# Kernel optimization log

Measured on AMD Instinct MI355X. Metric: run time of the kernel, lower is better.

The kernel has to match this reference:

```python
import jax, jax.numpy as jnp
import numpy as np

B, S, E, H = 4, 2048, 1024, 16
D = E // H  # head_dim = 64


def setup_inputs() -> dict:
    key = jax.random.key(0)
    k1, k2, k3, k4, k5 = jax.random.split(key, 5)
    # xavier_uniform bounds
    lim_qkv = float(np.sqrt(6.0 / (E + 3 * E)))
    lim_out = float(np.sqrt(6.0 / (E + E)))
    return {
        "inp": jax.random.normal(k1, (B, S, E), dtype=jnp.float32),
        "qkv_w": jax.random.uniform(k2, (3 * E, E), minval=-lim_qkv, maxval=lim_qkv, dtype=jnp.float32),
        "qkv_b": jnp.zeros((3 * E,), dtype=jnp.float32),
        "out_w": jax.random.uniform(k3, (E, E), minval=-lim_out, maxval=lim_out, dtype=jnp.float32),
        "out_b": jnp.zeros((E,), dtype=jnp.float32),
    }


def reference(inp, qkv_w, qkv_b, out_w, out_b):
    b, s, _ = inp.shape
    # qkv projection: [b,s,3E]
    qkv = jnp.einsum("bse,fe->bsf", inp, qkv_w) + qkv_b
    qkv = qkv.reshape(b, s, 3, H, D).transpose(2, 0, 3, 1, 4)  # [3,b,h,s,d]
    q, k, v = qkv[0], qkv[1], qkv[2]
    scale = 1.0 / jnp.sqrt(jnp.float32(D))
    scores = jnp.einsum("bhqd,bhkd->bhqk", q, k) * scale
    attn = jax.nn.softmax(scores, axis=-1)  # dropout = identity (eval mode)
    ctx = jnp.einsum("bhqk,bhkd->bhqd", attn, v)
    ctx = ctx.transpose(0, 2, 1, 3).reshape(b, s, E)
    out = jnp.einsum("bse,fe->bsf", ctx, out_w) + out_b
    return out
```

## Files before the change

### kernel.cpp

```cpp
#include <hip/hip_runtime.h>
#include <stdint.h>

typedef unsigned short u16;
typedef __bf16 bf16x8 __attribute__((ext_vector_type(8)));
typedef float f32x4 __attribute__((ext_vector_type(4)));
typedef float f32x16 __attribute__((ext_vector_type(16)));

#define DEV static __device__ __forceinline__

DEV u16 f2bf(float f) {
  uint32_t u = __float_as_uint(f);
  u += 0x7fffu + ((u >> 16) & 1u);
  return (u16)(u >> 16);
}

DEV void g2l16(const void* g, void* l) {
  __builtin_amdgcn_global_load_lds(
      (__attribute__((address_space(1))) void*)(g),
      (__attribute__((address_space(3))) void*)(l), 16, 0, 0);
}

DEV f32x4 mfma16(bf16x8 a, bf16x8 b, f32x4 c) {
  return __builtin_amdgcn_mfma_f32_16x16x32_bf16(a, b, c, 0, 0, 0);
}
DEV f32x16 mfma32(bf16x8 a, bf16x8 b, f32x16 c) {
  return __builtin_amdgcn_mfma_f32_32x32x16_bf16(a, b, c, 0, 0, 0);
}

DEV bf16x8 lds_ld(const char* p) { return *(const bf16x8*)p; }

DEV float fexp2(float x) {
  float r;
  asm("v_exp_f32 %0, %1" : "=v"(r) : "v"(x));
  return r;
}

DEV uint32_t cvtpk(float lo, float hi) {
  uint32_t r;
  asm("v_cvt_pk_bf16_f32 %0, %1, %2" : "=v"(r) : "v"(lo), "v"(hi));
  return r;
}
DEV void pswap(uint32_t& a, uint32_t& b) {
  auto r = __builtin_amdgcn_permlane32_swap((int)a, (int)b, false, false);
  a = (uint32_t)r[0];
  b = (uint32_t)r[1];
}
DEV float xhalf_sum(float x) {
  auto r = __builtin_amdgcn_permlane32_swap(__float_as_int(x), __float_as_int(x), false, false);
  return __int_as_float(r[0]) + __int_as_float(r[1]);
}

__global__ __launch_bounds__(256) void cvt_kernel(const float* __restrict__ in,
                                                  u16* __restrict__ out, int n4) {
  int i = blockIdx.x * 256 + threadIdx.x;
  if (i >= n4) return;
  float4 v = ((const float4*)in)[i];
  ushort4 o;
  o.x = f2bf(v.x); o.y = f2bf(v.y); o.z = f2bf(v.z); o.w = f2bf(v.w);
  ((ushort4*)out)[i] = o;
}

template<int EPI>
__global__ __launch_bounds__(256, 2) void gemm_bt(
    const u16* __restrict__ A, const u16* __restrict__ B,
    const float* __restrict__ bias, void* __restrict__ C,
    u16* __restrict__ vT,
    int M, int N, int K, int qcols, float qscale, int vcol0) {
  __shared__ char sm[2][32768];
  const int tid = threadIdx.x;
  const int w = tid >> 6, l = tid & 63;
  const int wr = w >> 1, wc = w & 1;
  const int bm0 = blockIdx.x * 128, bn0 = blockIdx.y * 128;
  const int lr = l >> 3, lsl = (l & 7) ^ lr;
  const u16* gA = A + (size_t)(bm0 + w * 32 + lr) * K + lsl * 8;
  const u16* gB = B + (size_t)(bn0 + w * 32 + lr) * K + lsl * 8;

  auto stage = [&](int t, int pp) {
    char* ba = sm[pp] + w * 32 * 128;
    char* bb = ba + 16384;
    const u16* a = gA + t * 64;
    const u16* b = gB + t * 64;
#pragma unroll
    for (int i = 0; i < 4; ++i) {
      g2l16(a + (size_t)i * 8 * K, ba + i * 8 * 128);
      g2l16(b + (size_t)i * 8 * K, bb + i * 8 * 128);
    }
  };

  f32x4 acc[4][4] = {};
  const int NT = K / 64;
  int pp = 0;
  stage(0, 0);
  __syncthreads();
  for (int t = 0; t < NT; ++t) {
    if (t + 1 < NT) stage(t + 1, pp ^ 1);
    const char* bufA = sm[pp];
    const char* bufB = bufA + 16384;
#pragma unroll
    for (int ks = 0; ks < 2; ++ks) {
      bf16x8 af[4], bfr[4];
#pragma unroll
      for (int i = 0; i < 4; ++i) {
        const int rowA = wr * 64 + i * 16 + (l & 15);
        const int colb = (ks * 64 + ((l >> 4) << 4)) ^ ((rowA & 7) << 4);
        af[i] = lds_ld(bufA + rowA * 128 + colb);
        const int rowB = wc * 64 + i * 16 + (l & 15);
        bfr[i] = lds_ld(bufB + rowB * 128 + colb);
      }
#pragma unroll
      for (int i = 0; i < 4; ++i)
#pragma unroll
        for (int j = 0; j < 4; ++j)
          acc[i][j] = mfma16(af[i], bfr[j], acc[i][j]);
    }
    __syncthreads();
    pp ^= 1;
  }
  const int cr = (l >> 4) * 4, cc = l & 15;
  if (EPI == 1 && bn0 >= vcol0) {
#pragma unroll
    for (int i = 0; i < 4; ++i) {
      const int gr = bm0 + wr * 64 + i * 16 + cr;
      const int b = gr >> 11, s = gr & 2047;
#pragma unroll
      for (int j = 0; j < 4; ++j) {
        const int gc = bn0 + wc * 64 + j * 16 + cc;
        const float bv = bias[gc];
        const int vc = gc - vcol0;
        u16* dst = vT + ((size_t)((b * 16 + (vc >> 6)) * 64 + (vc & 63))) * 2048 + s;
        ushort4 pk;
        pk.x = f2bf(acc[i][j][0] + bv);
        pk.y = f2bf(acc[i][j][1] + bv);
        pk.z = f2bf(acc[i][j][2] + bv);
        pk.w = f2bf(acc[i][j][3] + bv);
        *(ushort4*)dst = pk;
      }
    }
    return;
  }
#pragma unroll
  for (int i = 0; i < 4; ++i) {
    const int gr = bm0 + wr * 64 + i * 16 + cr;
#pragma unroll
    for (int j = 0; j < 4; ++j) {
      const int gc = bn0 + wc * 64 + j * 16 + cc;
      const float bv = bias[gc];
      const float scl = (gc < qcols) ? qscale : 1.0f;
#pragma unroll
      for (int r = 0; r < 4; ++r) {
        const float v = (acc[i][j][r] + bv) * scl;
        if (EPI == 0) ((float*)C)[(size_t)(gr + r) * N + gc] = v;
        else          ((u16*)C)[(size_t)(gr + r) * N + gc] = f2bf(v);
      }
    }
  }
}

__global__ __launch_bounds__(256, 2) void attn(const u16* __restrict__ qkv,
                                               const u16* __restrict__ vT,
                                               u16* __restrict__ ctx) {
  constexpr int S = 2048, E = 1024, TE = 3072, NT = S / 64;
  const int id = blockIdx.x;
  const int x = id & 7, j = id >> 3;
  const int bh = x * 8 + (j & 7), qt = j >> 3;
  const int b = bh >> 4, h = bh & 15;
  const int tid = threadIdx.x, w = tid >> 6, l = tid & 63;
  const int q = l & 31, hi = l >> 5;
  __shared__ char sm[2][16384];

  const int qglobA = qt * 256 + w * 64 + q;
  const int qglobB = qglobA + 32;
  const u16* qpA = qkv + (size_t)(b * S + qglobA) * TE + h * 64 + hi * 8;
  const u16* qpB = qkv + (size_t)(b * S + qglobB) * TE + h * 64 + hi * 8;
  bf16x8 qfA[4], qfB[4];
#pragma unroll
  for (int d = 0; d < 4; ++d) {
    qfA[d] = *(const bf16x8*)(qpA + d * 16);
    qfB[d] = *(const bf16x8*)(qpB + d * 16);
  }

  const int lr = l >> 3, lsl = (l & 7) ^ lr;
  const u16* gK = qkv + (size_t)(b * S) * TE + E + h * 64 + lsl * 8;
  const u16* gV = vT + (size_t)(bh * 64) * S + lsl * 8;

  auto stage = [&](int t, int pp) {
    char* bk = sm[pp] + w * 2048;
#pragma unroll
    for (int i = 0; i < 2; ++i) {
      const int row = w * 16 + i * 8 + lr;
      g2l16(gK + (size_t)(t * 64 + row) * TE, bk + i * 1024);
      g2l16(gV + (size_t)row * S + t * 64, bk + 8192 + i * 1024);
    }
  };

  f32x16 o0A = {}, o1A = {}, o0B = {}, o1B = {};
  float lsumA = 0.f, lsumB = 0.f;

  auto expsum = [&](f32x16& e, float& ls) {
    float ts[4] = {0.f, 0.f, 0.f, 0.f};
#pragma unroll
    for (int r = 0; r < 16; ++r) {
      e[r] = fexp2(e[r]);
      ts[r & 3] += e[r];
    }
    ls += (ts[0] + ts[1]) + (ts[2] + ts[3]);
  };
  auto mkfrag = [&](const f32x16& e, bf16x8& P0, bf16x8& P1) {
    uint32_t a0 = cvtpk(e[0], e[1]), c0 = cvtpk(e[4], e[5]);
    uint32_t a1 = cvtpk(e[2], e[3]), c1 = cvtpk(e[6], e[7]);
    pswap(a0, c0); pswap(a1, c1);
    uint32_t a2 = cvtpk(e[8], e[9]), c2 = cvtpk(e[12], e[13]);
    uint32_t a3 = cvtpk(e[10], e[11]), c3 = cvtpk(e[14], e[15]);
    pswap(a2, c2); pswap(a3, c3);
    union { uint32_t u[4]; bf16x8 v; } t0, t1;
    t0.u[0] = a0; t0.u[1] = a1; t0.u[2] = c0; t0.u[3] = c1;
    t1.u[0] = a2; t1.u[1] = a3; t1.u[2] = c2; t1.u[3] = c3;
    P0 = t0.v; P1 = t1.v;
  };

  int pp = 0;
  stage(0, 0);
  __syncthreads();
  for (int t = 0; t < NT; ++t) {
    if (t + 1 < NT) stage(t + 1, pp ^ 1);
    const char* bK = sm[pp];
    const char* bV = sm[pp] + 8192;
    const int swz = (q & 7) << 4;
#pragma unroll
    for (int s = 0; s < 2; ++s) {
      const char* kr = bK + (s * 32 + q) * 128;
      bf16x8 kf[4];
#pragma unroll
      for (int d = 0; d < 4; ++d) kf[d] = lds_ld(kr + (((d * 2 + hi) << 4) ^ swz));
      f32x16 stA = {}, stB = {};
      __builtin_amdgcn_s_setprio(1);
#pragma unroll
      for (int d = 0; d < 4; ++d) {
        stA = mfma32(kf[d], qfA[d], stA);
        stB = mfma32(kf[d], qfB[d], stB);
      }
      __builtin_amdgcn_s_setprio(0);
      const int s0 = (((s * 4 + hi) << 4) ^ swz);
      const int s1 = (((s * 4 + 2 + hi) << 4) ^ swz);
      const bf16x8 va0 = lds_ld(bV + q * 128 + s0);
      const bf16x8 va1 = lds_ld(bV + q * 128 + s1);
      const bf16x8 vb0 = lds_ld(bV + (32 + q) * 128 + s0);
      const bf16x8 vb1 = lds_ld(bV + (32 + q) * 128 + s1);
      expsum(stA, lsumA);
      expsum(stB, lsumB);
      bf16x8 pA0, pA1, pB0, pB1;
      mkfrag(stA, pA0, pA1);
      mkfrag(stB, pB0, pB1);
      __builtin_amdgcn_s_setprio(1);
      o0A = mfma32(va0, pA0, o0A); o0B = mfma32(va0, pB0, o0B);
      o0A = mfma32(va1, pA1, o0A); o0B = mfma32(va1, pB1, o0B);
      o1A = mfma32(vb0, pA0, o1A); o1B = mfma32(vb0, pB0, o1B);
      o1A = mfma32(vb1, pA1, o1A); o1B = mfma32(vb1, pB1, o1B);
      __builtin_amdgcn_s_setprio(0);
    }
    __syncthreads();
    pp ^= 1;
  }
  auto writeo = [&](const f32x16& e0, const f32x16& e1, float ls, int qg) {
    const float inv = 1.0f / xhalf_sum(ls);
    u16* cp = ctx + (size_t)(b * S + qg) * E + h * 64 + 4 * hi;
#pragma unroll
    for (int g = 0; g < 4; ++g) {
      ushort4 pk0, pk1;
      pk0.x = f2bf(e0[4 * g + 0] * inv); pk0.y = f2bf(e0[4 * g + 1] * inv);
      pk0.z = f2bf(e0[4 * g + 2] * inv); pk0.w = f2bf(e0[4 * g + 3] * inv);
      *(ushort4*)(cp + 8 * g) = pk0;
      pk1.x = f2bf(e1[4 * g + 0] * inv); pk1.y = f2bf(e1[4 * g + 1] * inv);
      pk1.z = f2bf(e1[4 * g + 2] * inv); pk1.w = f2bf(e1[4 * g + 3] * inv);
      *(ushort4*)(cp + 32 + 8 * g) = pk1;
    }
  };
  writeo(o0A, o1A, lsumA, qglobA);
  writeo(o0B, o1B, lsumB, qglobB);
}

extern "C" void kernel_launch(void* const* d_in, const int* in_sizes, int n_in,
                              void* d_out, int out_size, void* d_ws, size_t ws_size,
                              hipStream_t stream) {
  (void)in_sizes; (void)n_in; (void)out_size;
  const float* inp   = (const float*)d_in[0];
  const float* qkv_w = (const float*)d_in[1];
  const float* qkv_b = (const float*)d_in[2];
  const float* out_w = (const float*)d_in[3];
  const float* out_b = (const float*)d_in[4];
  char* ws = (char*)d_ws;
  if (ws_size < 92274688u) return;

  u16* inp_b  = (u16*)(ws);
  u16* qkvw_b = (u16*)(ws + 16777216);
  u16* outw_b = (u16*)(ws + 23068672);
  u16* qkvo   = (u16*)(ws + 25165824);
  u16* vTb    = (u16*)(ws + 75497472);
  u16* ctx    = inp_b;

  const float cexp = 0.18033688f;

  hipLaunchKernelGGL(cvt_kernel, dim3(8192), dim3(256), 0, stream, inp, inp_b, 2097152);
  hipLaunchKernelGGL(cvt_kernel, dim3(3072), dim3(256), 0, stream, qkv_w, qkvw_b, 786432);
  hipLaunchKernelGGL(cvt_kernel, dim3(1024), dim3(256), 0, stream, out_w, outw_b, 262144);
  hipLaunchKernelGGL((gemm_bt<1>), dim3(64, 24), dim3(256), 0, stream,
                     inp_b, qkvw_b, qkv_b, (void*)qkvo, vTb,
                     8192, 3072, 1024, 1024, cexp, 2048);
  hipLaunchKernelGGL(attn, dim3(512), dim3(256), 0, stream, qkvo, vTb, ctx);
  hipLaunchKernelGGL((gemm_bt<0>), dim3(64, 8), dim3(256), 0, stream,
                     ctx, outw_b, out_b, d_out, (u16*)nullptr,
                     8192, 1024, 1024, 0, 1.0f, 1 << 30);
}
```

Baseline: 171.6 us.

## Use 256x128 GEMM tiles with 8 waves and triple-buffered LDS pipeline

```diff
diff --git a/kernel.cpp b/kernel.cpp
--- a/kernel.cpp
+++ b/kernel.cpp
@@ -61,51 +61,56 @@
 }
 
 template<int EPI>
-__global__ __launch_bounds__(256, 2) void gemm_bt(
+__global__ __launch_bounds__(512, 2) void gemm256(
     const u16* __restrict__ A, const u16* __restrict__ B,
     const float* __restrict__ bias, void* __restrict__ C,
     u16* __restrict__ vT,
     int M, int N, int K, int qcols, float qscale, int vcol0) {
-  __shared__ char sm[2][32768];
+  __shared__ char sm[147456];
   const int tid = threadIdx.x;
   const int w = tid >> 6, l = tid & 63;
-  const int wr = w >> 1, wc = w & 1;
-  const int bm0 = blockIdx.x * 128, bn0 = blockIdx.y * 128;
+  const int wm = w >> 1, wn = w & 1;
+  const int bm0 = blockIdx.x * 256, bn0 = blockIdx.y * 128;
   const int lr = l >> 3, lsl = (l & 7) ^ lr;
-  const u16* gA = A + (size_t)(bm0 + w * 32 + lr) * K + lsl * 8;
-  const u16* gB = B + (size_t)(bn0 + w * 32 + lr) * K + lsl * 8;
-
-  auto stage = [&](int t, int pp) {
-    char* ba = sm[pp] + w * 32 * 128;
-    char* bb = ba + 16384;
+  const u16* gA = A + (size_t)(bm0 + w * 8 + lr) * K + lsl * 8;
+  const u16* gB = B + (size_t)(bn0 + w * 8 + lr) * K + lsl * 8;
+
+  auto stage = [&](int t) {
+    char* base = sm + (t % 3) * 49152 + w * 1024;
     const u16* a = gA + t * 64;
     const u16* b = gB + t * 64;
 #pragma unroll
-    for (int i = 0; i < 4; ++i) {
-      g2l16(a + (size_t)i * 8 * K, ba + i * 8 * 128);
-      g2l16(b + (size_t)i * 8 * K, bb + i * 8 * 128);
-    }
+    for (int r = 0; r < 4; ++r)
+      g2l16(a + (size_t)(r * 64) * K, base + r * 8192);
+#pragma unroll
+    for (int r = 0; r < 2; ++r)
+      g2l16(b + (size_t)(r * 64) * K, base + 32768 + r * 8192);
   };
 
   f32x4 acc[4][4] = {};
   const int NT = K / 64;
-  int pp = 0;
-  stage(0, 0);
-  __syncthreads();
+  stage(0); stage(1);
+  asm volatile("s_waitcnt vmcnt(6)" ::: "memory");
+  __builtin_amdgcn_s_barrier();
+  __builtin_amdgcn_sched_barrier(0);
   for (int t = 0; t < NT; ++t) {
-    if (t + 1 < NT) stage(t + 1, pp ^ 1);
-    const char* bufA = sm[pp];
-    const char* bufB = bufA + 16384;
+    if (t + 2 < NT) stage(t + 2);
+    const char* bufA = sm + (t % 3) * 49152;
+    const char* bufB = bufA + 32768;
 #pragma unroll
     for (int ks = 0; ks < 2; ++ks) {
       bf16x8 af[4], bfr[4];
 #pragma unroll
       for (int i = 0; i < 4; ++i) {
-        const int rowA = wr * 64 + i * 16 + (l & 15);
-        const int colb = (ks * 64 + ((l >> 4) << 4)) ^ ((rowA & 7) << 4);
-        af[i] = lds_ld(bufA + rowA * 128 + colb);
-        const int rowB = wc * 64 + i * 16 + (l & 15);
-        bfr[i] = lds_ld(bufB + rowB * 128 + colb);
+        const int rowA = wm * 64 + i * 16 + (l & 15);
+        af[i] = lds_ld(bufA + rowA * 128 +
+                       ((ks * 64 + ((l >> 4) << 4)) ^ ((rowA & 7) << 4)));
+      }
+#pragma unroll
+      for (int j = 0; j < 4; ++j) {
+        const int rowB = wn * 64 + j * 16 + (l & 15);
+        bfr[j] = lds_ld(bufB + rowB * 128 +
+                        ((ks * 64 + ((l >> 4) << 4)) ^ ((rowB & 7) << 4)));
       }
 #pragma unroll
       for (int i = 0; i < 4; ++i)
@@ -113,18 +118,25 @@
         for (int j = 0; j < 4; ++j)
           acc[i][j] = mfma16(af[i], bfr[j], acc[i][j]);
     }
-    __syncthreads();
-    pp ^= 1;
+    if (t + 2 < NT) {
+      asm volatile("s_waitcnt vmcnt(6)" ::: "memory");
+    } else if (t + 1 < NT) {
+      asm volatile("s_waitcnt vmcnt(0)" ::: "memory");
+    }
+    if (t + 1 < NT) {
+      __builtin_amdgcn_s_barrier();
+      __builtin_amdgcn_sched_barrier(0);
+    }
   }
   const int cr = (l >> 4) * 4, cc = l & 15;
   if (EPI == 1 && bn0 >= vcol0) {
 #pragma unroll
     for (int i = 0; i < 4; ++i) {
-      const int gr = bm0 + wr * 64 + i * 16 + cr;
+      const int gr = bm0 + wm * 64 + i * 16 + cr;
       const int b = gr >> 11, s = gr & 2047;
 #pragma unroll
       for (int j = 0; j < 4; ++j) {
-        const int gc = bn0 + wc * 64 + j * 16 + cc;
+        const int gc = bn0 + wn * 64 + j * 16 + cc;
         const float bv = bias[gc];
         const int vc = gc - vcol0;
         u16* dst = vT + ((size_t)((b * 16 + (vc >> 6)) * 64 + (vc & 63))) * 2048 + s;
@@ -140,10 +152,10 @@
   }
 #pragma unroll
   for (int i = 0; i < 4; ++i) {
-    const int gr = bm0 + wr * 64 + i * 16 + cr;
+    const int gr = bm0 + wm * 64 + i * 16 + cr;
 #pragma unroll
     for (int j = 0; j < 4; ++j) {
-      const int gc = bn0 + wc * 64 + j * 16 + cc;
+      const int gc = bn0 + wn * 64 + j * 16 + cc;
       const float bv = bias[gc];
       const float scl = (gc < qcols) ? qscale : 1.0f;
 #pragma unroll
@@ -303,11 +315,11 @@
   hipLaunchKernelGGL(cvt_kernel, dim3(8192), dim3(256), 0, stream, inp, inp_b, 2097152);
   hipLaunchKernelGGL(cvt_kernel, dim3(3072), dim3(256), 0, stream, qkv_w, qkvw_b, 786432);
   hipLaunchKernelGGL(cvt_kernel, dim3(1024), dim3(256), 0, stream, out_w, outw_b, 262144);
-  hipLaunchKernelGGL((gemm_bt<1>), dim3(64, 24), dim3(256), 0, stream,
+  hipLaunchKernelGGL((gemm256<1>), dim3(32, 24), dim3(512), 0, stream,
                      inp_b, qkvw_b, qkv_b, (void*)qkvo, vTb,
                      8192, 3072, 1024, 1024, cexp, 2048);
   hipLaunchKernelGGL(attn, dim3(512), dim3(256), 0, stream, qkvo, vTb, ctx);
-  hipLaunchKernelGGL((gemm_bt<0>), dim3(64, 8), dim3(256), 0, stream,
+  hipLaunchKernelGGL((gemm256<0>), dim3(32, 8), dim3(512), 0, stream,
                      ctx, outw_b, out_b, d_out, (u16*)nullptr,
                      8192, 1024, 1024, 0, 1.0f, 1 << 30);
 }
```

New measurement: 176.7 us. 1.03x slower.

## Halve per-warp query rows in attention to raise occupancy

Applied to the files above, without the earlier changes.

```diff
diff --git a/kernel.cpp b/kernel.cpp
--- a/kernel.cpp
+++ b/kernel.cpp
@@ -156,7 +156,7 @@
   }
 }
 
-__global__ __launch_bounds__(256, 2) void attn(const u16* __restrict__ qkv,
+__global__ __launch_bounds__(256, 4) void attn(const u16* __restrict__ qkv,
                                                const u16* __restrict__ vT,
                                                u16* __restrict__ ctx) {
   constexpr int S = 2048, E = 1024, TE = 3072, NT = S / 64;
@@ -168,16 +168,11 @@
   const int q = l & 31, hi = l >> 5;
   __shared__ char sm[2][16384];
 
-  const int qglobA = qt * 256 + w * 64 + q;
-  const int qglobB = qglobA + 32;
-  const u16* qpA = qkv + (size_t)(b * S + qglobA) * TE + h * 64 + hi * 8;
-  const u16* qpB = qkv + (size_t)(b * S + qglobB) * TE + h * 64 + hi * 8;
-  bf16x8 qfA[4], qfB[4];
-#pragma unroll
-  for (int d = 0; d < 4; ++d) {
-    qfA[d] = *(const bf16x8*)(qpA + d * 16);
-    qfB[d] = *(const bf16x8*)(qpB + d * 16);
-  }
+  const int qglob = qt * 128 + w * 32 + q;
+  const u16* qp = qkv + (size_t)(b * S + qglob) * TE + h * 64 + hi * 8;
+  bf16x8 qf[4];
+#pragma unroll
+  for (int d = 0; d < 4; ++d) qf[d] = *(const bf16x8*)(qp + d * 16);
 
   const int lr = l >> 3, lsl = (l & 7) ^ lr;
   const u16* gK = qkv + (size_t)(b * S) * TE + E + h * 64 + lsl * 8;
@@ -193,8 +188,8 @@
     }
   };
 
-  f32x16 o0A = {}, o1A = {}, o0B = {}, o1B = {};
-  float lsumA = 0.f, lsumB = 0.f;
+  f32x16 o0 = {}, o1 = {};
+  float lsum = 0.f;
 
   auto expsum = [&](f32x16& e, float& ls) {
     float ts[4] = {0.f, 0.f, 0.f, 0.f};
@@ -232,13 +227,10 @@
       bf16x8 kf[4];
 #pragma unroll
       for (int d = 0; d < 4; ++d) kf[d] = lds_ld(kr + (((d * 2 + hi) << 4) ^ swz));
-      f32x16 stA = {}, stB = {};
+      f32x16 st = {};
       __builtin_amdgcn_s_setprio(1);
 #pragma unroll
-      for (int d = 0; d < 4; ++d) {
-        stA = mfma32(kf[d], qfA[d], stA);
-        stB = mfma32(kf[d], qfB[d], stB);
-      }
+      for (int d = 0; d < 4; ++d) st = mfma32(kf[d], qf[d], st);
       __builtin_amdgcn_s_setprio(0);
       const int s0 = (((s * 4 + hi) << 4) ^ swz);
       const int s1 = (((s * 4 + 2 + hi) << 4) ^ swz);
@@ -246,37 +238,31 @@
       const bf16x8 va1 = lds_ld(bV + q * 128 + s1);
       const bf16x8 vb0 = lds_ld(bV + (32 + q) * 128 + s0);
       const bf16x8 vb1 = lds_ld(bV + (32 + q) * 128 + s1);
-      expsum(stA, lsumA);
-      expsum(stB, lsumB);
-      bf16x8 pA0, pA1, pB0, pB1;
-      mkfrag(stA, pA0, pA1);
-      mkfrag(stB, pB0, pB1);
+      expsum(st, lsum);
+      bf16x8 p0, p1;
+      mkfrag(st, p0, p1);
       __builtin_amdgcn_s_setprio(1);
-      o0A = mfma32(va0, pA0, o0A); o0B = mfma32(va0, pB0, o0B);
-      o0A = mfma32(va1, pA1, o0A); o0B = mfma32(va1, pB1, o0B);
-      o1A = mfma32(vb0, pA0, o1A); o1B = mfma32(vb0, pB0, o1B);
-      o1A = mfma32(vb1, pA1, o1A); o1B = mfma32(vb1, pB1, o1B);
+      o0 = mfma32(va0, p0, o0);
+      o0 = mfma32(va1, p1, o0);
+      o1 = mfma32(vb0, p0, o1);
+      o1 = mfma32(vb1, p1, o1);
       __builtin_amdgcn_s_setprio(0);
     }
     __syncthreads();
     pp ^= 1;
   }
-  auto writeo = [&](const f32x16& e0, const f32x16& e1, float ls, int qg) {
-    const float inv = 1.0f / xhalf_sum(ls);
-    u16* cp = ctx + (size_t)(b * S + qg) * E + h * 64 + 4 * hi;
-#pragma unroll
-    for (int g = 0; g < 4; ++g) {
-      ushort4 pk0, pk1;
-      pk0.x = f2bf(e0[4 * g + 0] * inv); pk0.y = f2bf(e0[4 * g + 1] * inv);
-      pk0.z = f2bf(e0[4 * g + 2] * inv); pk0.w = f2bf(e0[4 * g + 3] * inv);
-      *(ushort4*)(cp + 8 * g) = pk0;
-      pk1.x = f2bf(e1[4 * g + 0] * inv); pk1.y = f2bf(e1[4 * g + 1] * inv);
-      pk1.z = f2bf(e1[4 * g + 2] * inv); pk1.w = f2bf(e1[4 * g + 3] * inv);
-      *(ushort4*)(cp + 32 + 8 * g) = pk1;
-    }
-  };
-  writeo(o0A, o1A, lsumA, qglobA);
-  writeo(o0B, o1B, lsumB, qglobB);
+  const float inv = 1.0f / xhalf_sum(lsum);
+  u16* cp = ctx + (size_t)(b * S + qglob) * E + h * 64 + 4 * hi;
+#pragma unroll
+  for (int g = 0; g < 4; ++g) {
+    ushort4 pk0, pk1;
+    pk0.x = f2bf(o0[4 * g + 0] * inv); pk0.y = f2bf(o0[4 * g + 1] * inv);
+    pk0.z = f2bf(o0[4 * g + 2] * inv); pk0.w = f2bf(o0[4 * g + 3] * inv);
+    *(ushort4*)(cp + 8 * g) = pk0;
+    pk1.x = f2bf(o1[4 * g + 0] * inv); pk1.y = f2bf(o1[4 * g + 1] * inv);
+    pk1.z = f2bf(o1[4 * g + 2] * inv); pk1.w = f2bf(o1[4 * g + 3] * inv);
+    *(ushort4*)(cp + 32 + 8 * g) = pk1;
+  }
 }
 
 extern "C" void kernel_launch(void* const* d_in, const int* in_sizes, int n_in,
@@ -306,7 +292,7 @@
   hipLaunchKernelGGL((gemm_bt<1>), dim3(64, 24), dim3(256), 0, stream,
                      inp_b, qkvw_b, qkv_b, (void*)qkvo, vTb,
                      8192, 3072, 1024, 1024, cexp, 2048);
-  hipLaunchKernelGGL(attn, dim3(512), dim3(256), 0, stream, qkvo, vTb, ctx);
+  hipLaunchKernelGGL(attn, dim3(1024), dim3(256), 0, stream, qkvo, vTb, ctx);
   hipLaunchKernelGGL((gemm_bt<0>), dim3(64, 8), dim3(256), 0, stream,
                      ctx, outw_b, out_b, d_out, (u16*)nullptr,
                      8192, 1024, 1024, 0, 1.0f, 1 << 30);
```

New measurement: 172.6 us. About the same (+0.6%).
